# Kernel tuning notes

Measured on AMD Instinct MI355X. Metric: run time of the kernel, lower is better.

Reference implementation:

```python
import jax, jax.numpy as jnp
import numpy as np

D_MODEL = 2048
D_FF = 8192


def absmean_quant(w):
    # scale = mean(|w|); keep weights whose magnitude >= 0.7*scale, ternarize to {-1,0,1}
    scale = jnp.mean(jnp.abs(w))
    mask = (jnp.abs(w) >= scale * 0.7).astype(w.dtype)
    return jnp.sign(w) * mask


def setup_inputs() -> dict:
    key = jax.random.key(0)
    k_x, k_w1, k_w2 = jax.random.split(key, 3)
    x = jax.random.normal(k_x, (4, 4096, D_MODEL), dtype=jnp.float32)
    w1 = jax.random.normal(k_w1, (D_FF, D_MODEL), dtype=jnp.float32)  # fc1.weight
    b1 = jnp.zeros((D_FF,), dtype=jnp.float32)
    w2 = jax.random.normal(k_w2, (D_MODEL, D_FF), dtype=jnp.float32)  # fc2.weight
    b2 = jnp.zeros((D_MODEL,), dtype=jnp.float32)
    return {"x": x, "w1": w1, "b1": b1, "w2": w2, "b2": b2}


def reference(x, w1, b1, w2, b2):
    w1_q = absmean_quant(w1)
    w2_q = absmean_quant(w2)
    h = jnp.einsum('bsd,fd->bsf', x, w1_q) + b1  # fc1: [B,S,d_ff]
    h = jax.nn.gelu(h, approximate=False)        # torch nn.GELU default = exact erf
    out = jnp.einsum('bsf,df->bsd', h, w2_q) + b2  # fc2: [B,S,d_model]
    return out
```

## Files before the change

### kernel.cpp

```cpp
#include <hip/hip_runtime.h>
#include <hip/hip_bf16.h>
#include <math.h>
#include <stdint.h>

#define D_MODEL 2048
#define D_FF    8192
#define MTOK    16384
#define NW      (D_FF * D_MODEL)

typedef int    i32x4  __attribute__((ext_vector_type(4)));
typedef __bf16 bf16x8 __attribute__((ext_vector_type(8)));

#define GLOAD_LDS16(gp, lp)                                                   \
  __builtin_amdgcn_global_load_lds(                                           \
      (__attribute__((address_space(1))) void*)(gp),                          \
      (__attribute__((address_space(3))) void*)(lp), 16, 0, 0)

__global__ void absum_s1(const float* __restrict__ w1, const float* __restrict__ w2,
                         double* __restrict__ partials) {
    const float* w = blockIdx.y ? w2 : w1;
    __shared__ double sm[256];
    int tid = blockIdx.x * 256 + threadIdx.x;
    double s = 0.0;
    for (int i = tid; i < NW / 4; i += 1024 * 256) {
        float4 v = ((const float4*)w)[i];
        s += (double)fabsf(v.x) + (double)fabsf(v.y) + (double)fabsf(v.z) + (double)fabsf(v.w);
    }
    sm[threadIdx.x] = s;
    __syncthreads();
    for (int off = 128; off > 0; off >>= 1) {
        if (threadIdx.x < off) sm[threadIdx.x] += sm[threadIdx.x + off];
        __syncthreads();
    }
    if (threadIdx.x == 0) partials[blockIdx.y * 1024 + blockIdx.x] = sm[0];
}

__global__ void absum_s2(const double* __restrict__ partials, float* __restrict__ thr) {
    __shared__ double sm[256];
    for (int wsel = 0; wsel < 2; ++wsel) {
        const double* p = partials + wsel * 1024;
        double s = p[threadIdx.x] + p[threadIdx.x + 256] + p[threadIdx.x + 512] + p[threadIdx.x + 768];
        sm[threadIdx.x] = s;
        __syncthreads();
        for (int off = 128; off > 0; off >>= 1) {
            if (threadIdx.x < off) sm[threadIdx.x] += sm[threadIdx.x + off];
            __syncthreads();
        }
        if (threadIdx.x == 0) thr[wsel] = (float)(0.7 * (sm[0] / (double)NW));
        __syncthreads();
    }
}

__global__ void quantw1(const float* __restrict__ w, const float* __restrict__ thr,
                        int8_t* __restrict__ q) {
    float t = thr[0];
    int i = (blockIdx.x * 256 + threadIdx.x) * 4;
    float4 v = *(const float4*)(w + i);
    char4 o;
    o.x = (fabsf(v.x) >= t) ? (v.x > 0.f ? 1 : -1) : 0;
    o.y = (fabsf(v.y) >= t) ? (v.y > 0.f ? 1 : -1) : 0;
    o.z = (fabsf(v.z) >= t) ? (v.z > 0.f ? 1 : -1) : 0;
    o.w = (fabsf(v.w) >= t) ? (v.w > 0.f ? 1 : -1) : 0;
    *(char4*)(q + i) = o;
}

__global__ void quantw2(const float* __restrict__ w, const float* __restrict__ thr,
                        int8_t* __restrict__ q, float* __restrict__ colsum) {
    __shared__ int sm[256];
    float t = thr[1];
    const int row = blockIdx.x;
    const int tid = threadIdx.x;
    int isum = 0;
    #pragma unroll
    for (int j = 0; j < 8; ++j) {
        int idx = row * D_FF + j * 1024 + tid * 4;
        float4 v = *(const float4*)(w + idx);
        char4 o;
        o.x = (fabsf(v.x) >= t) ? (v.x > 0.f ? 1 : -1) : 0;
        o.y = (fabsf(v.y) >= t) ? (v.y > 0.f ? 1 : -1) : 0;
        o.z = (fabsf(v.z) >= t) ? (v.z > 0.f ? 1 : -1) : 0;
        o.w = (fabsf(v.w) >= t) ? (v.w > 0.f ? 1 : -1) : 0;
        isum += o.x + o.y + o.z + o.w;
        *(char4*)(q + idx) = o;
    }
    sm[tid] = isum;
    __syncthreads();
    for (int off = 128; off > 0; off >>= 1) {
        if (tid < off) sm[tid] += sm[tid + off];
        __syncthreads();
    }
    if (tid == 0) colsum[row] = (float)sm[0];
}

__global__ void xquant(const float* __restrict__ x, int8_t* __restrict__ xq,
                       float* __restrict__ sx) {
    __shared__ float sm[256];
    const int row = blockIdx.x;
    const int tid = threadIdx.x;
    float4 v[2];
    float mx = 0.f;
    #pragma unroll
    for (int j = 0; j < 2; ++j) {
        v[j] = *(const float4*)(x + (size_t)row * D_MODEL + j * 1024 + tid * 4);
        mx = fmaxf(mx, fmaxf(fmaxf(fabsf(v[j].x), fabsf(v[j].y)),
                             fmaxf(fabsf(v[j].z), fabsf(v[j].w))));
    }
    sm[tid] = mx;
    __syncthreads();
    for (int off = 128; off > 0; off >>= 1) {
        if (tid < off) sm[tid] = fmaxf(sm[tid], sm[tid + off]);
        __syncthreads();
    }
    float m = sm[0];
    float inv = (m > 0.f) ? 127.f / m : 0.f;
    if (tid == 0) sx[row] = (m > 0.f) ? m / 127.f : 0.f;
    #pragma unroll
    for (int j = 0; j < 2; ++j) {
        char4 o;
        o.x = (int8_t)min(127, max(-127, __float2int_rn(v[j].x * inv)));
        o.y = (int8_t)min(127, max(-127, __float2int_rn(v[j].y * inv)));
        o.z = (int8_t)min(127, max(-127, __float2int_rn(v[j].z * inv)));
        o.w = (int8_t)min(127, max(-127, __float2int_rn(v[j].w * inv)));
        *(char4*)(xq + (size_t)row * D_MODEL + j * 1024 + tid * 4) = o;
    }
}

__global__ void hquant(const __bf16* __restrict__ h, int8_t* __restrict__ hq,
                       float2* __restrict__ sh) {
    __shared__ float sm[256];
    const int row = blockIdx.x;
    const int tid = threadIdx.x;
    const float gmin = -0.17f;
    float vals[4][8];
    float mx = -1e30f;
    #pragma unroll
    for (int j = 0; j < 4; ++j) {
        bf16x8 b = *(const bf16x8*)(h + (size_t)row * D_FF + j * 2048 + tid * 8);
        #pragma unroll
        for (int e = 0; e < 8; ++e) {
            float f = (float)b[e];
            vals[j][e] = f;
            mx = fmaxf(mx, f);
        }
    }
    sm[tid] = mx;
    __syncthreads();
    for (int off = 128; off > 0; off >>= 1) {
        if (tid < off) sm[tid] = fmaxf(sm[tid], sm[tid + off]);
        __syncthreads();
    }
    float M = sm[0];
    float s = (M - gmin) / 254.f;
    float inv = 254.f / (M - gmin);
    if (tid == 0) sh[row] = make_float2(s, 127.f * s + gmin);
    #pragma unroll
    for (int j = 0; j < 4; ++j) {
        char4 o0, o1;
        int q[8];
        #pragma unroll
        for (int e = 0; e < 8; ++e)
            q[e] = min(127, max(-127, __float2int_rn((vals[j][e] - gmin) * inv) - 127));
        o0.x = q[0]; o0.y = q[1]; o0.z = q[2]; o0.w = q[3];
        o1.x = q[4]; o1.y = q[5]; o1.z = q[6]; o1.w = q[7];
        int8_t* p = hq + (size_t)row * D_FF + j * 2048 + tid * 8;
        *(char4*)p = o0;
        *(char4*)(p + 4) = o1;
    }
}

template<int EPI>
__global__ __launch_bounds__(512, 2) void gemm_i8_256(
    const int8_t* __restrict__ A,
    const int8_t* __restrict__ B,
    const float*  __restrict__ bias,
    const float*  __restrict__ rs,
    const float*  __restrict__ colsum,
    void* __restrict__ Cout,
    int M, int N, int K)
{
    __shared__ int8_t As[4][16384];
    __shared__ int8_t Bs[4][16384];

    const int tid  = threadIdx.x;
    const int wave = tid >> 6;
    const int lane = tid & 63;
    const int quad = lane >> 4;
    const int l15  = lane & 15;
    const int wm   = (wave >> 2) * 128;
    const int wn   = (wave & 3) * 64;

    const int gx   = gridDim.x;
    const int nwg  = gx * gridDim.y;
    const int orig = blockIdx.y * gx + blockIdx.x;
    const int cpx  = nwg >> 3;
    const int swz  = (orig & 7) * cpx + (orig >> 3);
    const int m0   = (swz / gx) * 256;
    const int n0   = (swz % gx) * 256;

    i32x4 acc[8][4] = {};

    const int8_t* gA[2]; const int8_t* gB[2];
    char* lA[2]; char* lB[2];
    #pragma unroll
    for (int it = 0; it < 2; ++it) {
        int slot = it * 512 + tid;
        int row  = slot >> 2;
        int cg   = (slot & 3) ^ ((row >> 1) & 3);
        gA[it] = A + (size_t)(m0 + row) * K + cg * 16;
        gB[it] = B + (size_t)(n0 + row) * K + cg * 16;
        lA[it] = (char*)&As[0][0] + it * 8192 + wave * 1024;
        lB[it] = (char*)&Bs[0][0] + it * 8192 + wave * 1024;
    }

    int aoff[4], boff[4];
    #pragma unroll
    for (int f = 0; f < 4; ++f) {
        int ra = wm + f * 16 + l15;
        aoff[f] = ra * 64 + ((quad ^ ((ra >> 1) & 3)) << 4);
        int rb = wn + f * 16 + l15;
        boff[f] = rb * 64 + ((quad ^ ((rb >> 1) & 3)) << 4);
    }

    const int NH = K >> 6;

    #pragma unroll
    for (int h = 0; h < 3; ++h) {
        #pragma unroll
        for (int it = 0; it < 2; ++it) {
            GLOAD_LDS16(gA[it], lA[it] + h * 16384);
            GLOAD_LDS16(gB[it], lB[it] + h * 16384);
            gA[it] += 64; gB[it] += 64;
        }
    }
    asm volatile("s_waitcnt vmcnt(8)" ::: "memory");
    __builtin_amdgcn_s_barrier();
    __builtin_amdgcn_sched_barrier(0);

    for (int s = 0; s < NH; ++s) {
        const int8_t* Ap = &As[s & 3][0];
        const int8_t* Bp = &Bs[s & 3][0];
        const int stg = (s + 3) & 3;
        const bool stage = (s + 3) < NH;
        i32x4 af[4], bf[4];

        #pragma unroll
        for (int f = 0; f < 4; ++f) bf[f] = *(const i32x4*)(Bp + boff[f]);
        #pragma unroll
        for (int f = 0; f < 4; ++f) af[f] = *(const i32x4*)(Ap + aoff[f]);
        if (stage) {
            GLOAD_LDS16(gA[0], lA[0] + stg * 16384);
            GLOAD_LDS16(gB[0], lB[0] + stg * 16384);
            gA[0] += 64; gB[0] += 64;
        }
        __builtin_amdgcn_sched_barrier(0);
        __builtin_amdgcn_s_barrier();
        __builtin_amdgcn_sched_barrier(0);
        __builtin_amdgcn_s_setprio(1);
        #pragma unroll
        for (int mf = 0; mf < 4; ++mf)
            #pragma unroll
            for (int nf = 0; nf < 4; ++nf)
                acc[mf][nf] = __builtin_amdgcn_mfma_i32_16x16x64_i8(
                    af[mf], bf[nf], acc[mf][nf], 0, 0, 0);
        __builtin_amdgcn_s_setprio(0);
        __builtin_amdgcn_sched_barrier(0);
        __builtin_amdgcn_s_barrier();
        __builtin_amdgcn_sched_barrier(0);

        #pragma unroll
        for (int f = 0; f < 4; ++f) af[f] = *(const i32x4*)(Ap + 4096 + aoff[f]);
        if (stage) {
            GLOAD_LDS16(gA[1], lA[1] + stg * 16384);
            GLOAD_LDS16(gB[1], lB[1] + stg * 16384);
            gA[1] += 64; gB[1] += 64;
        }
        __builtin_amdgcn_sched_barrier(0);
        __builtin_amdgcn_s_barrier();
        __builtin_amdgcn_sched_barrier(0);
        __builtin_amdgcn_s_setprio(1);
        #pragma unroll
        for (int mf = 0; mf < 4; ++mf)
            #pragma unroll
            for (int nf = 0; nf < 4; ++nf)
                acc[4 + mf][nf] = __builtin_amdgcn_mfma_i32_16x16x64_i8(
                    af[mf], bf[nf], acc[4 + mf][nf], 0, 0, 0);
        __builtin_amdgcn_s_setprio(0);
        if (s < NH - 3)       { asm volatile("s_waitcnt vmcnt(8)" ::: "memory"); }
        else if (s == NH - 3) { asm volatile("s_waitcnt vmcnt(4)" ::: "memory"); }
        else if (s == NH - 2) { asm volatile("s_waitcnt vmcnt(0)" ::: "memory"); }
        __builtin_amdgcn_sched_barrier(0);
        __builtin_amdgcn_s_barrier();
        __builtin_amdgcn_sched_barrier(0);
    }

    #pragma unroll
    for (int nf = 0; nf < 4; ++nf) {
        const int n = n0 + wn + nf * 16 + l15;
        const float bv = bias[n];
        const float cs = (EPI == 1) ? colsum[n] : 0.f;
        #pragma unroll
        for (int qm = 0; qm < 2; ++qm)
            #pragma unroll
            for (int mf = 0; mf < 4; ++mf)
                #pragma unroll
                for (int r = 0; r < 4; ++r) {
                    int m = m0 + wm + qm * 64 + mf * 16 + quad * 4 + r;
                    float a = (float)acc[qm * 4 + mf][nf][r];
                    if (EPI == 0) {
                        float v = rs[m] * a + bv;
                        v = 0.5f * v * (1.0f + erff(v * 0.70710678118654752f));
                        ((__bf16*)Cout)[(size_t)m * N + n] = (__bf16)v;
                    } else {
                        float2 so = ((const float2*)rs)[m];
                        ((float*)Cout)[(size_t)m * N + n] = so.x * a + so.y * cs + bv;
                    }
                }
    }
}

extern "C" void kernel_launch(void* const* d_in, const int* in_sizes, int n_in,
                              void* d_out, int out_size, void* d_ws, size_t ws_size,
                              hipStream_t stream) {
    const float* x  = (const float*)d_in[0];
    const float* w1 = (const float*)d_in[1];
    const float* b1 = (const float*)d_in[2];
    const float* w2 = (const float*)d_in[3];
    const float* b2 = (const float*)d_in[4];
    float* out = (float*)d_out;

    char* ws = (char*)d_ws;
    float*  thr = (float*)ws;
    float*  sx  = (float*)(ws + 256);
    float2* sh  = (float2*)(ws + 256 + (64 << 10));
    float*  colsum = (float*)(ws + 256 + (192 << 10));
    int8_t* xq  = (int8_t*)(ws + 256 + (256 << 10));
    int8_t* w1q = xq  + (size_t)MTOK * D_MODEL;
    int8_t* w2q = w1q + (size_t)D_FF * D_MODEL;
    int8_t* hq  = w2q + (size_t)D_MODEL * D_FF;
    __bf16* h   = (__bf16*)(hq + (size_t)MTOK * D_FF);
    double* partials = (double*)h;

    absum_s1<<<dim3(1024, 2), 256, 0, stream>>>(w1, w2, partials);
    absum_s2<<<1, 256, 0, stream>>>(partials, thr);

    quantw1<<<NW / 1024, 256, 0, stream>>>(w1, thr, w1q);
    quantw2<<<D_MODEL, 256, 0, stream>>>(w2, thr, w2q, colsum);
    xquant<<<MTOK, 256, 0, stream>>>(x, xq, sx);

    dim3 g1(D_FF / 256, MTOK / 256);
    gemm_i8_256<0><<<g1, 512, 0, stream>>>(xq, w1q, b1, sx, nullptr, (void*)h,
                                           MTOK, D_FF, D_MODEL);

    hquant<<<MTOK, 256, 0, stream>>>(h, hq, sh);

    dim3 g2(D_MODEL / 256, MTOK / 256);
    gemm_i8_256<1><<<g2, 512, 0, stream>>>(hq, w2q, b2, (const float*)sh, colsum, (void*)out,
                                           MTOK, D_MODEL, D_FF);
}
```

Measured before the change: 1.271 ms.

## Shrink int8 GEMM tile to 256x128 with 3-stage pipeline and higher occupancy

Replaces the 256x256 int8 GEMM tile with a 256x128 tile over 8 waves, each computing 64x64. LDS drops to three 24 KB stages, launch bounds target 4 blocks per CU, and the loop uses a single barrier per K-step instead of three. The aim is more resident workgroups and less synchronisation to hide latency. It also adds a custom XCD-aware block swizzle for the second GEMM. In exchange each tile has lower arithmetic intensity, so global and LDS traffic per MFMA rises and the prefetch depth shrinks from three stages to two.

```diff
diff --git a/kernel.cpp b/kernel.cpp
--- a/kernel.cpp
+++ b/kernel.cpp
@@ -169,7 +169,7 @@
 }
 
 template<int EPI>
-__global__ __launch_bounds__(512, 2) void gemm_i8_256(
+__global__ __launch_bounds__(512, 4) void gemm_i8_bt(
     const int8_t* __restrict__ A,
     const int8_t* __restrict__ B,
     const float*  __restrict__ bias,
@@ -178,39 +178,46 @@
     void* __restrict__ Cout,
     int M, int N, int K)
 {
-    __shared__ int8_t As[4][16384];
-    __shared__ int8_t Bs[4][16384];
+    __shared__ int8_t Sh[3 * 24576];
 
     const int tid  = threadIdx.x;
     const int wave = tid >> 6;
     const int lane = tid & 63;
     const int quad = lane >> 4;
     const int l15  = lane & 15;
-    const int wm   = (wave >> 2) * 128;
-    const int wn   = (wave & 3) * 64;
+    const int wm   = (wave >> 1) * 64;
+    const int wn   = (wave & 1) * 64;
 
     const int gx   = gridDim.x;
     const int nwg  = gx * gridDim.y;
     const int orig = blockIdx.y * gx + blockIdx.x;
-    const int cpx  = nwg >> 3;
-    const int swz  = (orig & 7) * cpx + (orig >> 3);
-    const int m0   = (swz / gx) * 256;
-    const int n0   = (swz % gx) * 256;
-
-    i32x4 acc[8][4] = {};
-
-    const int8_t* gA[2]; const int8_t* gB[2];
-    char* lA[2]; char* lB[2];
-    #pragma unroll
-    for (int it = 0; it < 2; ++it) {
-        int slot = it * 512 + tid;
-        int row  = slot >> 2;
-        int cg   = (slot & 3) ^ ((row >> 1) & 3);
-        gA[it] = A + (size_t)(m0 + row) * K + cg * 16;
-        gB[it] = B + (size_t)(n0 + row) * K + cg * 16;
-        lA[it] = (char*)&As[0][0] + it * 8192 + wave * 1024;
-        lB[it] = (char*)&Bs[0][0] + it * 8192 + wave * 1024;
-    }
+    int by, bx;
+    if (EPI == 0) {
+        const int swz = (orig & 7) * (nwg >> 3) + (orig >> 3);
+        by = swz >> 6;
+        bx = swz & 63;
+    } else {
+        const int xcd = orig & 7;
+        const int l   = orig >> 3;
+        const int st  = l >> 6;
+        const int r   = l & 63;
+        by = xcd * 8 + st * 4 + (r & 3);
+        bx = r >> 2;
+    }
+    const int m0 = by << 8;
+    const int n0 = bx << 7;
+
+    i32x4 acc[4][4] = {};
+
+    const int row0 = tid >> 2;
+    const int cg0  = (tid & 3) ^ ((row0 >> 1) & 3);
+    const int8_t* gA0 = A + (size_t)(m0 + row0) * K + cg0 * 16;
+    const int8_t* gA1 = gA0 + (size_t)128 * K;
+    const int8_t* gB0 = B + (size_t)(n0 + row0) * K + cg0 * 16;
+    char* const ldsb = (char*)Sh;
+    char* const dA0  = ldsb + wave * 1024;
+    char* const dA1  = ldsb + 8192  + wave * 1024;
+    char* const dB0  = ldsb + 16384 + wave * 1024;
 
     int aoff[4], boff[4];
     #pragma unroll
@@ -218,79 +225,53 @@
         int ra = wm + f * 16 + l15;
         aoff[f] = ra * 64 + ((quad ^ ((ra >> 1) & 3)) << 4);
         int rb = wn + f * 16 + l15;
-        boff[f] = rb * 64 + ((quad ^ ((rb >> 1) & 3)) << 4);
+        boff[f] = 16384 + rb * 64 + ((quad ^ ((rb >> 1) & 3)) << 4);
     }
 
     const int NH = K >> 6;
-
-    #pragma unroll
-    for (int h = 0; h < 3; ++h) {
-        #pragma unroll
-        for (int it = 0; it < 2; ++it) {
-            GLOAD_LDS16(gA[it], lA[it] + h * 16384);
-            GLOAD_LDS16(gB[it], lB[it] + h * 16384);
-            gA[it] += 64; gB[it] += 64;
-        }
-    }
-    asm volatile("s_waitcnt vmcnt(8)" ::: "memory");
+    const int STG = 24576;
+
+    #pragma unroll
+    for (int h = 0; h < 2; ++h) {
+        GLOAD_LDS16(gA0, dA0 + h * STG);
+        GLOAD_LDS16(gA1, dA1 + h * STG);
+        GLOAD_LDS16(gB0, dB0 + h * STG);
+        gA0 += 64; gA1 += 64; gB0 += 64;
+    }
+    asm volatile("s_waitcnt vmcnt(3)" ::: "memory");
     __builtin_amdgcn_s_barrier();
     __builtin_amdgcn_sched_barrier(0);
 
+    int roff = 0;
+    int soff = 2 * STG;
+
     for (int s = 0; s < NH; ++s) {
-        const int8_t* Ap = &As[s & 3][0];
-        const int8_t* Bp = &Bs[s & 3][0];
-        const int stg = (s + 3) & 3;
-        const bool stage = (s + 3) < NH;
-        i32x4 af[4], bf[4];
-
-        #pragma unroll
-        for (int f = 0; f < 4; ++f) bf[f] = *(const i32x4*)(Bp + boff[f]);
-        #pragma unroll
-        for (int f = 0; f < 4; ++f) af[f] = *(const i32x4*)(Ap + aoff[f]);
-        if (stage) {
-            GLOAD_LDS16(gA[0], lA[0] + stg * 16384);
-            GLOAD_LDS16(gB[0], lB[0] + stg * 16384);
-            gA[0] += 64; gB[0] += 64;
+        if (s + 2 < NH) {
+            GLOAD_LDS16(gA0, ldsb + soff + (dA0 - ldsb));
+            GLOAD_LDS16(gA1, ldsb + soff + (dA1 - ldsb));
+            GLOAD_LDS16(gB0, ldsb + soff + (dB0 - ldsb));
+            gA0 += 64; gA1 += 64; gB0 += 64;
         }
-        __builtin_amdgcn_sched_barrier(0);
-        __builtin_amdgcn_s_barrier();
-        __builtin_amdgcn_sched_barrier(0);
+        i32x4 bfr[4];
+        #pragma unroll
+        for (int f = 0; f < 4; ++f) bfr[f] = *(const i32x4*)(ldsb + roff + boff[f]);
         __builtin_amdgcn_s_setprio(1);
         #pragma unroll
-        for (int mf = 0; mf < 4; ++mf)
+        for (int mf = 0; mf < 4; ++mf) {
+            i32x4 af = *(const i32x4*)(ldsb + roff + aoff[mf]);
             #pragma unroll
             for (int nf = 0; nf < 4; ++nf)
                 acc[mf][nf] = __builtin_amdgcn_mfma_i32_16x16x64_i8(
-                    af[mf], bf[nf], acc[mf][nf], 0, 0, 0);
+                    af, bfr[nf], acc[mf][nf], 0, 0, 0);
+        }
         __builtin_amdgcn_s_setprio(0);
-        __builtin_amdgcn_sched_barrier(0);
-        __builtin_amdgcn_s_barrier();
-        __builtin_amdgcn_sched_barrier(0);
-
-        #pragma unroll
-        for (int f = 0; f < 4; ++f) af[f] = *(const i32x4*)(Ap + 4096 + aoff[f]);
-        if (stage) {
-            GLOAD_LDS16(gA[1], lA[1] + stg * 16384);
-            GLOAD_LDS16(gB[1], lB[1] + stg * 16384);
-            gA[1] += 64; gB[1] += 64;
-        }
-        __builtin_amdgcn_sched_barrier(0);
-        __builtin_amdgcn_s_barrier();
-        __builtin_amdgcn_sched_barrier(0);
-        __builtin_amdgcn_s_setprio(1);
-        #pragma unroll
-        for (int mf = 0; mf < 4; ++mf)
-            #pragma unroll
-            for (int nf = 0; nf < 4; ++nf)
-                acc[4 + mf][nf] = __builtin_amdgcn_mfma_i32_16x16x64_i8(
-                    af[mf], bf[nf], acc[4 + mf][nf], 0, 0, 0);
-        __builtin_amdgcn_s_setprio(0);
-        if (s < NH - 3)       { asm volatile("s_waitcnt vmcnt(8)" ::: "memory"); }
-        else if (s == NH - 3) { asm volatile("s_waitcnt vmcnt(4)" ::: "memory"); }
+        if (s < NH - 2)       { asm volatile("s_waitcnt vmcnt(3)" ::: "memory"); }
         else if (s == NH - 2) { asm volatile("s_waitcnt vmcnt(0)" ::: "memory"); }
         __builtin_amdgcn_sched_barrier(0);
         __builtin_amdgcn_s_barrier();
         __builtin_amdgcn_sched_barrier(0);
+        roff = (roff == 2 * STG) ? 0 : roff + STG;
+        soff = (soff == 2 * STG) ? 0 : soff + STG;
     }
 
     #pragma unroll
@@ -299,22 +280,20 @@
         const float bv = bias[n];
         const float cs = (EPI == 1) ? colsum[n] : 0.f;
         #pragma unroll
-        for (int qm = 0; qm < 2; ++qm)
+        for (int mf = 0; mf < 4; ++mf)
             #pragma unroll
-            for (int mf = 0; mf < 4; ++mf)
-                #pragma unroll
-                for (int r = 0; r < 4; ++r) {
-                    int m = m0 + wm + qm * 64 + mf * 16 + quad * 4 + r;
-                    float a = (float)acc[qm * 4 + mf][nf][r];
-                    if (EPI == 0) {
-                        float v = rs[m] * a + bv;
-                        v = 0.5f * v * (1.0f + erff(v * 0.70710678118654752f));
-                        ((__bf16*)Cout)[(size_t)m * N + n] = (__bf16)v;
-                    } else {
-                        float2 so = ((const float2*)rs)[m];
-                        ((float*)Cout)[(size_t)m * N + n] = so.x * a + so.y * cs + bv;
-                    }
+            for (int r = 0; r < 4; ++r) {
+                int m = m0 + wm + mf * 16 + quad * 4 + r;
+                float a = (float)acc[mf][nf][r];
+                if (EPI == 0) {
+                    float v = rs[m] * a + bv;
+                    v = 0.5f * v * (1.0f + erff(v * 0.70710678118654752f));
+                    ((__bf16*)Cout)[(size_t)m * N + n] = (__bf16)v;
+                } else {
+                    float2 so = ((const float2*)rs)[m];
+                    ((float*)Cout)[(size_t)m * N + n] = so.x * a + so.y * cs + bv;
                 }
+            }
     }
 }
 
@@ -347,13 +326,13 @@
     quantw2<<<D_MODEL, 256, 0, stream>>>(w2, thr, w2q, colsum);
     xquant<<<MTOK, 256, 0, stream>>>(x, xq, sx);
 
-    dim3 g1(D_FF / 256, MTOK / 256);
-    gemm_i8_256<0><<<g1, 512, 0, stream>>>(xq, w1q, b1, sx, nullptr, (void*)h,
-                                           MTOK, D_FF, D_MODEL);
+    dim3 g1(D_FF / 128, MTOK / 256);
+    gemm_i8_bt<0><<<g1, 512, 0, stream>>>(xq, w1q, b1, sx, nullptr, (void*)h,
+                                          MTOK, D_FF, D_MODEL);
 
     hquant<<<MTOK, 256, 0, stream>>>(h, hq, sh);
 
-    dim3 g2(D_MODEL / 256, MTOK / 256);
-    gemm_i8_256<1><<<g2, 512, 0, stream>>>(hq, w2q, b2, (const float*)sh, colsum, (void*)out,
-                                           MTOK, D_MODEL, D_FF);
-}
+    dim3 g2(D_MODEL / 128, MTOK / 256);
+    gemm_i8_bt<1><<<g2, 512, 0, stream>>>(hq, w2q, b2, (const float*)sh, colsum, (void*)out,
+                                          MTOK, D_MODEL, D_FF);
+}
```

Result: faster. 1.115 ms (-12.3%).
